# Kernel optimization log

Measured on AMD Instinct MI355X. Metric: run time of the kernel, lower is better.

## Reference

```python
import jax, jax.numpy as jnp
from jax import lax
import numpy as np

NUM_TAGS = 48
START = NUM_TAGS
STOP = NUM_TAGS + 1
LABEL_SMOOTHING = 0.1
NEG = -10000.0


def setup_inputs() -> dict:
    key = jax.random.key(0)
    k1, k2, k3 = jax.random.split(key, 3)
    B, T = 1024, 512
    emissions = jax.random.normal(k1, (B, T, NUM_TAGS), dtype=jnp.float32)
    tags = jax.random.randint(k2, (B, T), 0, NUM_TAGS, dtype=jnp.int64)
    mask = jnp.ones((B, T), dtype=bool)
    # learned transitions, initialized as in the torch module
    trans = jax.random.normal(k3, (NUM_TAGS + 2, NUM_TAGS + 2), dtype=jnp.float32) * 0.1
    trans = trans.at[:, START].set(NEG)          # never transition into START
    trans = trans.at[STOP, :].set(NEG)           # never transition out of STOP
    trans = trans.at[0, 0].add(-2.0)             # TAG2IDX.get('O', 0) == 0
    return {"emissions": emissions, "tags": tags, "mask": mask, "transitions": trans}


def _crf_nll(emissions, transitions, tags, mask):
    B, T, K = emissions.shape
    # ---- forward algorithm (log partition) ----
    alpha0 = jnp.full((B, K + 2), NEG, dtype=emissions.dtype).at[:, START].set(0.0)

    def step(alpha, inp):
        emit, m = inp                                   # emit: [B,K], m: [B]
        # sc[b,j] = logsumexp_i(alpha[b,i] + transitions[i,j])
        sc = jax.nn.logsumexp(alpha[:, :, None] + transitions[None], axis=1)  # [B,K+2]
        sc = sc.at[:, :K].add(emit)
        alpha = jnp.where(m[:, None], sc, alpha)
        return alpha, None

    alpha, _ = lax.scan(step, alpha0,
                        (jnp.swapaxes(emissions, 0, 1), jnp.swapaxes(mask, 0, 1)))
    log_z = jax.nn.logsumexp(alpha[:, :K] + transitions[:K, STOP][None], axis=1)  # [B]

    # ---- gold score ----
    mf = mask.astype(emissions.dtype)
    emit_g = jnp.take_along_axis(emissions, tags[..., None], axis=2)[..., 0]  # [B,T]
    gold = (transitions[START, tags[:, 0]]
            + jnp.sum(emit_g * mf, axis=1)
            + jnp.sum(transitions[tags[:, :-1], tags[:, 1:]] * mf[:, 1:], axis=1))
    last = jnp.sum(mask.astype(jnp.int32), axis=1) - 1                        # [B]
    last_tags = jnp.take_along_axis(tags, last[:, None].astype(tags.dtype), axis=1)[:, 0]
    gold = gold + transitions[last_tags, STOP]

    nll = jnp.mean(log_z - gold)
    h_max = jnp.log(jnp.asarray(K + 1e-12, dtype=nll.dtype))
    return (1.0 - LABEL_SMOOTHING) * nll + LABEL_SMOOTHING * h_max


def reference(emissions, tags, mask, transitions):
    return _crf_nll(emissions, transitions, tags, mask)
```

## Files before the change

kernel.cpp:

```cpp
#include <hip/hip_runtime.h>
#include <hip/hip_bf16.h>
#include <math.h>


#define NTAGS   48
#define NST     50
#define START_S 48
#define STOP_S  49
#define BATCH   1024
#define TLEN    512

typedef short  bf16x8 __attribute__((ext_vector_type(8)));
typedef float  f32x4  __attribute__((ext_vector_type(4)));

union B4 { unsigned u[4]; short s[8]; bf16x8 v; };

__device__ __forceinline__ short to_bf16(float f) {
    unsigned u = __float_as_uint(f);
    unsigned r = ((u >> 16) & 1u) + 0x7FFFu;
    return (short)((u + r) >> 16);
}

__device__ __forceinline__ unsigned pk2(float lo, float hi) {
    float2 f; f.x = lo; f.y = hi;
    __hip_bfloat162 h = __float22bfloat162_rn(f);
    union { __hip_bfloat162 h; unsigned u; } cvt; cvt.h = h;
    return cvt.u;
}

__device__ __forceinline__ float wave_sum(float v) {
#pragma unroll
    for (int off = 32; off >= 1; off >>= 1)
        v += __shfl_xor(v, off, 64);
    return v;
}

__device__ __forceinline__ void gload_lds16(const float* g, f32x4* l) {
    __builtin_amdgcn_global_load_lds(
        (const __attribute__((address_space(1))) unsigned int*)(const void*)g,
        (__attribute__((address_space(3))) unsigned int*)(void*)l,
        16, 0, 0);
}

#define VMWAIT24 asm volatile("s_waitcnt vmcnt(24)" ::: "memory");

#define RENORM_APPLY                                                     \
    {   int ex = ((rbp >> 23) & 255) - 127;                              \
        ex = ex > 126 ? 126 : (ex < -126 ? -126 : ex);                   \
        float sc = __uint_as_float((unsigned)(127 - ex) << 23);          \
        p0 *= sc; p1 *= sc; p2 *= sc;                                    \
        Clog += (float)ex * 0.69314718055994531f; }

template<int MODE, int LAST>
__device__ __forceinline__ void fwd_step(const bf16x8 (&A)[3][2],
    bf16x8 &B0, bf16x8 &B1,
    const f32x4 &X0, const f32x4 &X1, const f32x4 &X2,
    f32x4 &p0, f32x4 &p1, f32x4 &p2, float &Clog, int bp_addr, int &rbp)
{
    const f32x4 z = {0.f, 0.f, 0.f, 0.f};
    f32x4 a0 = __builtin_amdgcn_mfma_f32_16x16x32_bf16(A[0][0], B0, z, 0, 0, 0);
    a0 = __builtin_amdgcn_mfma_f32_16x16x32_bf16(A[0][1], B1, a0, 0, 0, 0);
    f32x4 a1 = __builtin_amdgcn_mfma_f32_16x16x32_bf16(A[1][0], B0, z, 0, 0, 0);
    a1 = __builtin_amdgcn_mfma_f32_16x16x32_bf16(A[1][1], B1, a1, 0, 0, 0);
    f32x4 a2 = __builtin_amdgcn_mfma_f32_16x16x32_bf16(A[2][0], B0, z, 0, 0, 0);
    a2 = __builtin_amdgcn_mfma_f32_16x16x32_bf16(A[2][1], B1, a2, 0, 0, 0);
    p0 = a0 * X0;  p1 = a1 * X1;  p2 = a2 * X2;
    if (MODE == 2) RENORM_APPLY
    if (MODE == 1) rbp = __builtin_amdgcn_ds_bpermute(bp_addr, __float_as_int(p0[0]));
    if (!LAST) {
        B4 nb0;
        nb0.u[0] = pk2(p0[0], p0[1]);  nb0.u[1] = pk2(p0[2], p0[3]);
        nb0.u[2] = pk2(p1[0], p1[1]);  nb0.u[3] = pk2(p1[2], p1[3]);
        B0 = nb0.v;
        B4 nb1;
        nb1.u[0] = pk2(p2[0], p2[1]);  nb1.u[1] = pk2(p2[2], p2[3]);
        nb1.u[2] = 0u;                 nb1.u[3] = 0u;
        B1 = nb1.v;
    }
}

template<int MODE>
__device__ __forceinline__ void bwd_step(const bf16x8 (&A)[3][2],
    const f32x4 &X0, const f32x4 &X1, const f32x4 &X2,
    f32x4 &p0, f32x4 &p1, f32x4 &p2, float &Clog, int bp_addr, int &rbp)
{
    f32x4 h0 = p0 * X0, h1 = p1 * X1, h2 = p2 * X2;
    B4 nb0;
    nb0.u[0] = pk2(h0[0], h0[1]);  nb0.u[1] = pk2(h0[2], h0[3]);
    nb0.u[2] = pk2(h1[0], h1[1]);  nb0.u[3] = pk2(h1[2], h1[3]);
    B4 nb1;
    nb1.u[0] = pk2(h2[0], h2[1]);  nb1.u[1] = pk2(h2[2], h2[3]);
    nb1.u[2] = 0u;                 nb1.u[3] = 0u;
    const bf16x8 B0 = nb0.v, B1 = nb1.v;
    const f32x4 z = {0.f, 0.f, 0.f, 0.f};
    f32x4 a0 = __builtin_amdgcn_mfma_f32_16x16x32_bf16(A[0][0], B0, z, 0, 0, 0);
    a0 = __builtin_amdgcn_mfma_f32_16x16x32_bf16(A[0][1], B1, a0, 0, 0, 0);
    f32x4 a1 = __builtin_amdgcn_mfma_f32_16x16x32_bf16(A[1][0], B0, z, 0, 0, 0);
    a1 = __builtin_amdgcn_mfma_f32_16x16x32_bf16(A[1][1], B1, a1, 0, 0, 0);
    f32x4 a2 = __builtin_amdgcn_mfma_f32_16x16x32_bf16(A[2][0], B0, z, 0, 0, 0);
    a2 = __builtin_amdgcn_mfma_f32_16x16x32_bf16(A[2][1], B1, a2, 0, 0, 0);
    p0 = a0;  p1 = a1;  p2 = a2;
    if (MODE == 2) RENORM_APPLY
    if (MODE == 1) rbp = __builtin_amdgcn_ds_bpermute(bp_addr, __float_as_int(p0[0]));
}

#define STAGE(BUF, T)                                                        \
    { const int tb_ = (T);                                                   \
      _Pragma("unroll") for (int u2 = 0; u2 < 4; ++u2)                       \
        _Pragma("unroll") for (int mt = 0; mt < 3; ++mt)                     \
            gload_lds16(emg + (size_t)(tb_ + u2) * NTAGS + 16 * mt,          \
                        &ldsb[BUF][u2 * 3 + mt][0]); }

#define STAGE_D(BUF, T)                                                      \
    { const int tb_ = (T);                                                   \
      _Pragma("unroll") for (int u2 = 0; u2 < 4; ++u2)                       \
        _Pragma("unroll") for (int mt = 0; mt < 3; ++mt)                     \
            gload_lds16(emg + (size_t)(tb_ - u2) * NTAGS + 16 * mt,          \
                        &ldsb[BUF][u2 * 3 + mt][0]); }

#define RDX(BUF, U2)                                                         \
    rw[U2][0] = ldsb[BUF][(U2) * 3 + 0][l];                                  \
    rw[U2][1] = ldsb[BUF][(U2) * 3 + 1][l];                                  \
    rw[U2][2] = ldsb[BUF][(U2) * 3 + 2][l];

#define EXX(EXN, U2)                                                         \
    _Pragma("unroll") for (int mt = 0; mt < 3; ++mt)                         \
        _Pragma("unroll") for (int r = 0; r < 4; ++r)                        \
            EXN[U2][mt][r] = __expf(rw[U2][mt][r]);

#define FSTEPS(EXC, EXN, BN, BS, T)                                          \
    fwd_step<0,0>(A, B0, B1, EXC[0][0], EXC[0][1], EXC[0][2], p0, p1, p2, Clog, bp_addr, rbp); \
    RDX(BN, 0)                                                               \
    fwd_step<0,0>(A, B0, B1, EXC[1][0], EXC[1][1], EXC[1][2], p0, p1, p2, Clog, bp_addr, rbp); \
    RDX(BN, 1) RDX(BN, 2)                                                    \
    { int ts_ = (T) + 16; if (ts_ > 253) ts_ = 253; STAGE(BS, ts_) }         \
    fwd_step<1,0>(A, B0, B1, EXC[2][0], EXC[2][1], EXC[2][2], p0, p1, p2, Clog, bp_addr, rbp); \
    RDX(BN, 3)                                                               \
    EXX(EXN, 0) EXX(EXN, 1)                                                  \
    fwd_step<2,0>(A, B0, B1, EXC[3][0], EXC[3][1], EXC[3][2], p0, p1, p2, Clog, bp_addr, rbp); \
    EXX(EXN, 2) EXX(EXN, 3)

#define BSTEPS(EXC, EXN, BN, BS, T)                                          \
    bwd_step<0>(A, EXC[0][0], EXC[0][1], EXC[0][2], p0, p1, p2, Clog, bp_addr, rbp); \
    RDX(BN, 0)                                                               \
    bwd_step<0>(A, EXC[1][0], EXC[1][1], EXC[1][2], p0, p1, p2, Clog, bp_addr, rbp); \
    RDX(BN, 1) RDX(BN, 2)                                                    \
    { int ts_ = (T) - 16; if (ts_ < 259) ts_ = 259; STAGE_D(BS, ts_) }       \
    bwd_step<1>(A, EXC[2][0], EXC[2][1], EXC[2][2], p0, p1, p2, Clog, bp_addr, rbp); \
    RDX(BN, 3)                                                               \
    EXX(EXN, 0) EXX(EXN, 1)                                                  \
    bwd_step<2>(A, EXC[3][0], EXC[3][1], EXC[3][2], p0, p1, p2, Clog, bp_addr, rbp); \
    EXX(EXN, 2) EXX(EXN, 3)

#define WS_Q    0
#define WS_U    49152
#define WS_CF   98304
#define WS_CB   99328
#define WS_GOLD 100352
#define WS_ACC  101376
#define WS_CNT  101377
#define WS_NEEDED_FLOATS 101378

__global__ __launch_bounds__(64)
__attribute__((amdgpu_waves_per_eu(1, 1)))
void crf_main(const float* __restrict__ emissions,
              const int*   __restrict__ tags,
              const float* __restrict__ trans,
              float*       __restrict__ ws)
{
    __shared__ __align__(16) f32x4 ldsb[4][12][64];
    const int bid = blockIdx.x;
    const int l = threadIdx.x;

    if (bid >= 128) {
        const int gb = bid - 128;
        for (int rr = 0; rr < 8; ++rr) {
            const int b = gb * 8 + rr;
            const float* em  = emissions + (size_t)b * TLEN * NTAGS;
            const int*   tbp = tags + (size_t)b * TLEN;
            float gacc = 0.0f;
#pragma unroll
            for (int k = 0; k < TLEN / 64; ++k) {
                const int tt  = k * 64 + l;
                const int tag = tbp[tt];
                gacc += em[(size_t)tt * NTAGS + tag];
                if (tt >= 1) gacc += trans[tbp[tt - 1] * NST + tag];
            }
            gacc = wave_sum(gacc);
            if (l == 0)
                ws[WS_GOLD + b] = gacc + trans[START_S * NST + tbp[0]]
                                       + trans[tbp[TLEN - 1] * NST + STOP_S];
        }
        return;
    }

    const bool is_fwd = (bid < 64);
    const int grp = is_fwd ? bid : (bid - 64);
    const int g = l >> 4;
    const int c = l & 15;
    const int brow = grp * 16 + c;

    bf16x8 A[3][2];
#pragma unroll
    for (int mt = 0; mt < 3; ++mt)
#pragma unroll
        for (int kt = 0; kt < 2; ++kt) {
            B4 u;
#pragma unroll
            for (int e = 0; e < 8; ++e) {
                const int sk = 16 * (2 * kt + (e >> 2)) + 4 * g + (e & 3);
                const int m  = 16 * mt + c;
                float f = 0.0f;
                if (sk < NTAGS)
                    f = __expf(is_fwd ? trans[sk * NST + m] : trans[m * NST + sk]);
                u.s[e] = to_bf16(f);
            }
            A[mt][kt] = u.v;
        }
    asm volatile("" : "+v"(A[0][0]), "+v"(A[0][1]), "+v"(A[1][0]),
                      "+v"(A[1][1]), "+v"(A[2][0]), "+v"(A[2][1]));

    const float* emc = emissions + (size_t)brow * (TLEN * NTAGS);
    const float* emg = emc + 4 * g;

    const int bp_addr = c << 2;
    f32x4 p0, p1, p2;
    float Clog = 0.0f;
    int rbp = __float_as_int(1.0f);
    f32x4 EXa[4][3], EXb[4][3], rw[4][3];

    if (is_fwd) {
        bf16x8 B0, B1;
        {
            f32x4 i0 = *(const f32x4*)(emc +      4 * g);
            f32x4 i1 = *(const f32x4*)(emc + 16 + 4 * g);
            f32x4 i2 = *(const f32x4*)(emc + 32 + 4 * g);
            B4 nb0, nb1;
#pragma unroll
            for (int r = 0; r < 4; ++r) {
                nb0.s[r]     = to_bf16(__expf(trans[START_S * NST +      4 * g + r] + i0[r]));
                nb0.s[4 + r] = to_bf16(__expf(trans[START_S * NST + 16 + 4 * g + r] + i1[r]));
                nb1.s[r]     = to_bf16(__expf(trans[START_S * NST + 32 + 4 * g + r] + i2[r]));
            }
            nb1.u[2] = 0u;  nb1.u[3] = 0u;
            B0 = nb0.v;  B1 = nb1.v;
        }
        STAGE(0, 1) STAGE(1, 5) STAGE(2, 9)
        VMWAIT24
        RDX(0, 0) RDX(0, 1) RDX(0, 2) RDX(0, 3)
        EXX(EXa, 0) EXX(EXa, 1) EXX(EXa, 2) EXX(EXa, 3)
        STAGE(3, 13)
        int t = 1, bi = 0;
        for (int pr = 0; pr < 31; ++pr) {
            VMWAIT24
            FSTEPS(EXa, EXb, (bi + 1) & 3, bi, t)
            t += 4; bi = (bi + 1) & 3;
            VMWAIT24
            FSTEPS(EXb, EXa, (bi + 1) & 3, bi, t)
            t += 4; bi = (bi + 1) & 3;
        }
        VMWAIT24
        FSTEPS(EXa, EXb, (bi + 1) & 3, bi, t)
        fwd_step<0,0>(A, B0, B1, EXb[0][0], EXb[0][1], EXb[0][2], p0, p1, p2, Clog, bp_addr, rbp);
        fwd_step<0,0>(A, B0, B1, EXb[1][0], EXb[1][1], EXb[1][2], p0, p1, p2, Clog, bp_addr, rbp);
        fwd_step<0,1>(A, B0, B1, EXb[2][0], EXb[2][1], EXb[2][2], p0, p1, p2, Clog, bp_addr, rbp);

        float* q = ws + WS_Q + (size_t)grp * 768 + l * 12;
#pragma unroll
        for (int r = 0; r < 4; ++r) {
            q[r] = p0[r];  q[4 + r] = p1[r];  q[8 + r] = p2[r];
        }
        if (g == 0) ws[WS_CF + grp * 16 + c] = Clog;
    } else {
#pragma unroll
        for (int r = 0; r < 4; ++r) {
            p0[r] = __expf(trans[(     4 * g + r) * NST + STOP_S]);
            p1[r] = __expf(trans[(16 + 4 * g + r) * NST + STOP_S]);
            p2[r] = __expf(trans[(32 + 4 * g + r) * NST + STOP_S]);
        }
        STAGE_D(0, 511) STAGE_D(1, 507) STAGE_D(2, 503)
        VMWAIT24
        RDX(0, 0) RDX(0, 1) RDX(0, 2) RDX(0, 3)
        EXX(EXa, 0) EXX(EXa, 1) EXX(EXa, 2) EXX(EXa, 3)
        STAGE_D(3, 499)
        int t = 511, bi = 0;
        for (int pr = 0; pr < 32; ++pr) {
            VMWAIT24
            BSTEPS(EXa, EXb, (bi + 1) & 3, bi, t)
            t -= 4; bi = (bi + 1) & 3;
            VMWAIT24
            BSTEPS(EXb, EXa, (bi + 1) & 3, bi, t)
            t -= 4; bi = (bi + 1) & 3;
        }
        float* u = ws + WS_U + (size_t)grp * 768 + l * 12;
#pragma unroll
        for (int r = 0; r < 4; ++r) {
            u[r] = p0[r];  u[4 + r] = p1[r];  u[8 + r] = p2[r];
        }
        if (g == 0) ws[WS_CB + grp * 16 + c] = Clog;
    }
}

__global__ __launch_bounds__(64)
void crf_combine(float* __restrict__ ws, float* __restrict__ out)
{
    const int grp = blockIdx.x;
    const int l = threadIdx.x;
    const float* q = ws + WS_Q + (size_t)grp * 768 + l * 12;
    const float* u = ws + WS_U + (size_t)grp * 768 + l * 12;
    float s = 0.0f;
#pragma unroll
    for (int k = 0; k < 12; ++k) s += q[k] * u[k];
    s += __shfl_xor(s, 16, 64);
    s += __shfl_xor(s, 32, 64);
    float v = 0.0f;
    if (l < 16) {
        const float logz = ws[WS_CF + grp * 16 + l]
                         + ws[WS_CB + grp * 16 + l] + __logf(s);
        v = logz - ws[WS_GOLD + grp * 16 + l];
    }
    v = wave_sum(v);
    if (l == 0) {
        atomicAdd(&ws[WS_ACC], v);
        __threadfence();
        unsigned old = atomicAdd((unsigned*)&ws[WS_CNT], 1u);
        if (old == 63u) {
            const float tot = atomicAdd(&ws[WS_ACC], 0.0f);
            const float nll = tot / (float)BATCH;
            out[0] = 0.9f * nll + 0.1f * logf((float)NTAGS);
        }
    }
}

extern "C" void kernel_launch(void* const* d_in, const int* in_sizes, int n_in,
                              void* d_out, int out_size, void* d_ws, size_t ws_size,
                              hipStream_t stream)
{
    const float* emissions = (const float*)d_in[0];
    const int*   tags      = (const int*)d_in[1];
    const float* trans     = (const float*)d_in[3];

    if (ws_size < WS_NEEDED_FLOATS * sizeof(float)) return;
    float* ws = (float*)d_ws;

    hipMemsetAsync(ws + WS_ACC, 0, 2 * sizeof(float), stream);

    crf_main<<<256, 64, 0, stream>>>(emissions, tags, trans, ws);
    crf_combine<<<64, 64, 0, stream>>>(ws, (float*)d_out);
}
```

Before: 74.11 us.

## Interleave two independent batch chains per wave in forward/backward recurrence

```diff
diff --git a/kernel.cpp b/kernel.cpp
--- a/kernel.cpp
+++ b/kernel.cpp
@@ -42,7 +42,7 @@
         16, 0, 0);
 }
 
-#define VMWAIT24 asm volatile("s_waitcnt vmcnt(24)" ::: "memory");
+#define VMWAIT48 asm volatile("s_waitcnt vmcnt(48)" ::: "memory");
 
 #define RENORM_APPLY                                                     \
     {   int ex = ((rbp >> 23) & 255) - 127;                              \
@@ -104,53 +104,63 @@
     if (MODE == 1) rbp = __builtin_amdgcn_ds_bpermute(bp_addr, __float_as_int(p0[0]));
 }
 
-#define STAGE(BUF, T)                                                        \
+#define STAGEC(C, BUF, T)                                                    \
     { const int tb_ = (T);                                                   \
       _Pragma("unroll") for (int u2 = 0; u2 < 4; ++u2)                       \
         _Pragma("unroll") for (int mt = 0; mt < 3; ++mt)                     \
-            gload_lds16(emg + (size_t)(tb_ + u2) * NTAGS + 16 * mt,          \
-                        &ldsb[BUF][u2 * 3 + mt][0]); }
-
-#define STAGE_D(BUF, T)                                                      \
+            gload_lds16(emg_[C] + (size_t)(tb_ + u2) * NTAGS + 16 * mt,      \
+                        &ldsb[C][BUF][u2 * 3 + mt][0]); }
+
+#define STAGEC_D(C, BUF, T)                                                  \
     { const int tb_ = (T);                                                   \
       _Pragma("unroll") for (int u2 = 0; u2 < 4; ++u2)                       \
         _Pragma("unroll") for (int mt = 0; mt < 3; ++mt)                     \
-            gload_lds16(emg + (size_t)(tb_ - u2) * NTAGS + 16 * mt,          \
-                        &ldsb[BUF][u2 * 3 + mt][0]); }
-
-#define RDX(BUF, U2)                                                         \
-    rw[U2][0] = ldsb[BUF][(U2) * 3 + 0][l];                                  \
-    rw[U2][1] = ldsb[BUF][(U2) * 3 + 1][l];                                  \
-    rw[U2][2] = ldsb[BUF][(U2) * 3 + 2][l];
-
-#define EXX(EXN, U2)                                                         \
+            gload_lds16(emg_[C] + (size_t)(tb_ - u2) * NTAGS + 16 * mt,      \
+                        &ldsb[C][BUF][u2 * 3 + mt][0]); }
+
+#define RDXC(C, BUF, U2)                                                     \
+    rw[C][U2][0] = ldsb[C][BUF][(U2) * 3 + 0][l];                            \
+    rw[C][U2][1] = ldsb[C][BUF][(U2) * 3 + 1][l];                            \
+    rw[C][U2][2] = ldsb[C][BUF][(U2) * 3 + 2][l];
+
+#define EXXC(C, EXN, U2)                                                     \
     _Pragma("unroll") for (int mt = 0; mt < 3; ++mt)                         \
         _Pragma("unroll") for (int r = 0; r < 4; ++r)                        \
-            EXN[U2][mt][r] = __expf(rw[U2][mt][r]);
-
-#define FSTEPS(EXC, EXN, BN, BS, T)                                          \
-    fwd_step<0,0>(A, B0, B1, EXC[0][0], EXC[0][1], EXC[0][2], p0, p1, p2, Clog, bp_addr, rbp); \
-    RDX(BN, 0)                                                               \
-    fwd_step<0,0>(A, B0, B1, EXC[1][0], EXC[1][1], EXC[1][2], p0, p1, p2, Clog, bp_addr, rbp); \
-    RDX(BN, 1) RDX(BN, 2)                                                    \
-    { int ts_ = (T) + 16; if (ts_ > 253) ts_ = 253; STAGE(BS, ts_) }         \
-    fwd_step<1,0>(A, B0, B1, EXC[2][0], EXC[2][1], EXC[2][2], p0, p1, p2, Clog, bp_addr, rbp); \
-    RDX(BN, 3)                                                               \
-    EXX(EXN, 0) EXX(EXN, 1)                                                  \
-    fwd_step<2,0>(A, B0, B1, EXC[3][0], EXC[3][1], EXC[3][2], p0, p1, p2, Clog, bp_addr, rbp); \
-    EXX(EXN, 2) EXX(EXN, 3)
-
-#define BSTEPS(EXC, EXN, BN, BS, T)                                          \
-    bwd_step<0>(A, EXC[0][0], EXC[0][1], EXC[0][2], p0, p1, p2, Clog, bp_addr, rbp); \
-    RDX(BN, 0)                                                               \
-    bwd_step<0>(A, EXC[1][0], EXC[1][1], EXC[1][2], p0, p1, p2, Clog, bp_addr, rbp); \
-    RDX(BN, 1) RDX(BN, 2)                                                    \
-    { int ts_ = (T) - 16; if (ts_ < 259) ts_ = 259; STAGE_D(BS, ts_) }       \
-    bwd_step<1>(A, EXC[2][0], EXC[2][1], EXC[2][2], p0, p1, p2, Clog, bp_addr, rbp); \
-    RDX(BN, 3)                                                               \
-    EXX(EXN, 0) EXX(EXN, 1)                                                  \
-    bwd_step<2>(A, EXC[3][0], EXC[3][1], EXC[3][2], p0, p1, p2, Clog, bp_addr, rbp); \
-    EXX(EXN, 2) EXX(EXN, 3)
+            EXN[C][U2][mt][r] = __expf(rw[C][U2][mt][r]);
+
+#define FSTEPC(C, MODE, LAST, EXC, S)                                        \
+    fwd_step<MODE, LAST>(A, B0_[C], B1_[C], EXC[C][S][0], EXC[C][S][1],      \
+        EXC[C][S][2], p0_[C], p1_[C], p2_[C], Clog_[C], bp_addr, rbp_[C]);
+
+#define BSTEPC(C, MODE, EXC, S)                                              \
+    bwd_step<MODE>(A, EXC[C][S][0], EXC[C][S][1], EXC[C][S][2],              \
+        p0_[C], p1_[C], p2_[C], Clog_[C], bp_addr, rbp_[C]);
+
+#define DFSTEPS(EXC, EXN, BN, BS, T)                                         \
+    FSTEPC(0,0,0,EXC,0) FSTEPC(1,0,0,EXC,0)                                  \
+    RDXC(0,BN,0) RDXC(1,BN,0)                                                \
+    FSTEPC(0,0,0,EXC,1) FSTEPC(1,0,0,EXC,1)                                  \
+    RDXC(0,BN,1) RDXC(1,BN,1) RDXC(0,BN,2) RDXC(1,BN,2)                      \
+    { int ts_ = (T) + 16; if (ts_ > 253) ts_ = 253;                          \
+      STAGEC(0,BS,ts_) STAGEC(1,BS,ts_) }                                    \
+    FSTEPC(0,1,0,EXC,2) FSTEPC(1,1,0,EXC,2)                                  \
+    RDXC(0,BN,3) RDXC(1,BN,3)                                                \
+    EXXC(0,EXN,0) EXXC(1,EXN,0) EXXC(0,EXN,1) EXXC(1,EXN,1)                  \
+    FSTEPC(0,2,0,EXC,3) FSTEPC(1,2,0,EXC,3)                                  \
+    EXXC(0,EXN,2) EXXC(1,EXN,2) EXXC(0,EXN,3) EXXC(1,EXN,3)
+
+#define DBSTEPS(EXC, EXN, BN, BS, T)                                         \
+    BSTEPC(0,0,EXC,0) BSTEPC(1,0,EXC,0)                                      \
+    RDXC(0,BN,0) RDXC(1,BN,0)                                                \
+    BSTEPC(0,0,EXC,1) BSTEPC(1,0,EXC,1)                                      \
+    RDXC(0,BN,1) RDXC(1,BN,1) RDXC(0,BN,2) RDXC(1,BN,2)                      \
+    { int ts_ = (T) - 16; if (ts_ < 259) ts_ = 259;                          \
+      STAGEC_D(0,BS,ts_) STAGEC_D(1,BS,ts_) }                                \
+    BSTEPC(0,1,EXC,2) BSTEPC(1,1,EXC,2)                                      \
+    RDXC(0,BN,3) RDXC(1,BN,3)                                                \
+    EXXC(0,EXN,0) EXXC(1,EXN,0) EXXC(0,EXN,1) EXXC(1,EXN,1)                  \
+    BSTEPC(0,2,EXC,3) BSTEPC(1,2,EXC,3)                                      \
+    EXXC(0,EXN,2) EXXC(1,EXN,2) EXXC(0,EXN,3) EXXC(1,EXN,3)
 
 #define WS_Q    0
 #define WS_U    49152
@@ -168,14 +178,12 @@
               const float* __restrict__ trans,
               float*       __restrict__ ws)
 {
-    __shared__ __align__(16) f32x4 ldsb[4][12][64];
+    __shared__ __align__(16) f32x4 ldsb[2][4][12][64];
     const int bid = blockIdx.x;
     const int l = threadIdx.x;
 
-    if (bid >= 128) {
-        const int gb = bid - 128;
-        for (int rr = 0; rr < 8; ++rr) {
-            const int b = gb * 8 + rr;
+    if (bid >= 64) {
+        for (int b = bid - 64; b < BATCH; b += 192) {
             const float* em  = emissions + (size_t)b * TLEN * NTAGS;
             const int*   tbp = tags + (size_t)b * TLEN;
             float gacc = 0.0f;
@@ -194,11 +202,10 @@
         return;
     }
 
-    const bool is_fwd = (bid < 64);
-    const int grp = is_fwd ? bid : (bid - 64);
+    const bool is_fwd = (bid < 32);
+    const int gbase = is_fwd ? (2 * bid) : (2 * (bid - 32));
     const int g = l >> 4;
     const int c = l & 15;
-    const int brow = grp * 16 + c;
 
     bf16x8 A[3][2];
 #pragma unroll
@@ -220,21 +227,27 @@
     asm volatile("" : "+v"(A[0][0]), "+v"(A[0][1]), "+v"(A[1][0]),
                       "+v"(A[1][1]), "+v"(A[2][0]), "+v"(A[2][1]));
 
-    const float* emc = emissions + (size_t)brow * (TLEN * NTAGS);
-    const float* emg = emc + 4 * g;
+    const float* emc_[2];
+    const float* emg_[2];
+#pragma unroll
+    for (int C = 0; C < 2; ++C) {
+        emc_[C] = emissions + (size_t)((gbase + C) * 16 + c) * (TLEN * NTAGS);
+        emg_[C] = emc_[C] + 4 * g;
+    }
 
     const int bp_addr = c << 2;
-    f32x4 p0, p1, p2;
-    float Clog = 0.0f;
-    int rbp = __float_as_int(1.0f);
-    f32x4 EXa[4][3], EXb[4][3], rw[4][3];
+    bf16x8 B0_[2], B1_[2];
+    f32x4 p0_[2], p1_[2], p2_[2];
+    float Clog_[2] = {0.0f, 0.0f};
+    int rbp_[2] = {0, 0};
+    f32x4 EXa[2][4][3], EXb[2][4][3], rw[2][4][3];
 
     if (is_fwd) {
-        bf16x8 B0, B1;
-        {
-            f32x4 i0 = *(const f32x4*)(emc +      4 * g);
-            f32x4 i1 = *(const f32x4*)(emc + 16 + 4 * g);
-            f32x4 i2 = *(const f32x4*)(emc + 32 + 4 * g);
+#pragma unroll
+        for (int C = 0; C < 2; ++C) {
+            f32x4 i0 = *(const f32x4*)(emc_[C] +      4 * g);
+            f32x4 i1 = *(const f32x4*)(emc_[C] + 16 + 4 * g);
+            f32x4 i2 = *(const f32x4*)(emc_[C] + 32 + 4 * g);
             B4 nb0, nb1;
 #pragma unroll
             for (int r = 0; r < 4; ++r) {
@@ -243,61 +256,75 @@
                 nb1.s[r]     = to_bf16(__expf(trans[START_S * NST + 32 + 4 * g + r] + i2[r]));
             }
             nb1.u[2] = 0u;  nb1.u[3] = 0u;
-            B0 = nb0.v;  B1 = nb1.v;
-        }
-        STAGE(0, 1) STAGE(1, 5) STAGE(2, 9)
-        VMWAIT24
-        RDX(0, 0) RDX(0, 1) RDX(0, 2) RDX(0, 3)
-        EXX(EXa, 0) EXX(EXa, 1) EXX(EXa, 2) EXX(EXa, 3)
-        STAGE(3, 13)
+            B0_[C] = nb0.v;  B1_[C] = nb1.v;
+        }
+        STAGEC(0,0,1) STAGEC(1,0,1) STAGEC(0,1,5) STAGEC(1,1,5)
+        STAGEC(0,2,9) STAGEC(1,2,9)
+        VMWAIT48
+        RDXC(0,0,0) RDXC(1,0,0) RDXC(0,0,1) RDXC(1,0,1)
+        RDXC(0,0,2) RDXC(1,0,2) RDXC(0,0,3) RDXC(1,0,3)
+        EXXC(0,EXa,0) EXXC(1,EXa,0) EXXC(0,EXa,1) EXXC(1,EXa,1)
+        EXXC(0,EXa,2) EXXC(1,EXa,2) EXXC(0,EXa,3) EXXC(1,EXa,3)
+        STAGEC(0,3,13) STAGEC(1,3,13)
         int t = 1, bi = 0;
         for (int pr = 0; pr < 31; ++pr) {
-            VMWAIT24
-            FSTEPS(EXa, EXb, (bi + 1) & 3, bi, t)
+            VMWAIT48
+            DFSTEPS(EXa, EXb, (bi + 1) & 3, bi, t)
             t += 4; bi = (bi + 1) & 3;
-            VMWAIT24
-            FSTEPS(EXb, EXa, (bi + 1) & 3, bi, t)
+            VMWAIT48
+            DFSTEPS(EXb, EXa, (bi + 1) & 3, bi, t)
             t += 4; bi = (bi + 1) & 3;
         }
-        VMWAIT24
-        FSTEPS(EXa, EXb, (bi + 1) & 3, bi, t)
-        fwd_step<0,0>(A, B0, B1, EXb[0][0], EXb[0][1], EXb[0][2], p0, p1, p2, Clog, bp_addr, rbp);
-        fwd_step<0,0>(A, B0, B1, EXb[1][0], EXb[1][1], EXb[1][2], p0, p1, p2, Clog, bp_addr, rbp);
-        fwd_step<0,1>(A, B0, B1, EXb[2][0], EXb[2][1], EXb[2][2], p0, p1, p2, Clog, bp_addr, rbp);
-
-        float* q = ws + WS_Q + (size_t)grp * 768 + l * 12;
-#pragma unroll
-        for (int r = 0; r < 4; ++r) {
-            q[r] = p0[r];  q[4 + r] = p1[r];  q[8 + r] = p2[r];
-        }
-        if (g == 0) ws[WS_CF + grp * 16 + c] = Clog;
+        VMWAIT48
+        DFSTEPS(EXa, EXb, (bi + 1) & 3, bi, t)
+        FSTEPC(0,0,0,EXb,0) FSTEPC(1,0,0,EXb,0)
+        FSTEPC(0,0,0,EXb,1) FSTEPC(1,0,0,EXb,1)
+        FSTEPC(0,0,1,EXb,2) FSTEPC(1,0,1,EXb,2)
+
+#pragma unroll
+        for (int C = 0; C < 2; ++C) {
+            float* q = ws + WS_Q + (size_t)(gbase + C) * 768 + l * 12;
+#pragma unroll
+            for (int r = 0; r < 4; ++r) {
+                q[r] = p0_[C][r];  q[4 + r] = p1_[C][r];  q[8 + r] = p2_[C][r];
+            }
+            if (g == 0) ws[WS_CF + (gbase + C) * 16 + c] = Clog_[C];
+        }
     } else {
 #pragma unroll
-        for (int r = 0; r < 4; ++r) {
-            p0[r] = __expf(trans[(     4 * g + r) * NST + STOP_S]);
-            p1[r] = __expf(trans[(16 + 4 * g + r) * NST + STOP_S]);
-            p2[r] = __expf(trans[(32 + 4 * g + r) * NST + STOP_S]);
-        }
-        STAGE_D(0, 511) STAGE_D(1, 507) STAGE_D(2, 503)
-        VMWAIT24
-        RDX(0, 0) RDX(0, 1) RDX(0, 2) RDX(0, 3)
-        EXX(EXa, 0) EXX(EXa, 1) EXX(EXa, 2) EXX(EXa, 3)
-        STAGE_D(3, 499)
+        for (int C = 0; C < 2; ++C)
+#pragma unroll
+            for (int r = 0; r < 4; ++r) {
+                p0_[C][r] = __expf(trans[(     4 * g + r) * NST + STOP_S]);
+                p1_[C][r] = __expf(trans[(16 + 4 * g + r) * NST + STOP_S]);
+                p2_[C][r] = __expf(trans[(32 + 4 * g + r) * NST + STOP_S]);
+            }
+        STAGEC_D(0,0,511) STAGEC_D(1,0,511) STAGEC_D(0,1,507) STAGEC_D(1,1,507)
+        STAGEC_D(0,2,503) STAGEC_D(1,2,503)
+        VMWAIT48
+        RDXC(0,0,0) RDXC(1,0,0) RDXC(0,0,1) RDXC(1,0,1)
+        RDXC(0,0,2) RDXC(1,0,2) RDXC(0,0,3) RDXC(1,0,3)
+        EXXC(0,EXa,0) EXXC(1,EXa,0) EXXC(0,EXa,1) EXXC(1,EXa,1)
+        EXXC(0,EXa,2) EXXC(1,EXa,2) EXXC(0,EXa,3) EXXC(1,EXa,3)
+        STAGEC_D(0,3,499) STAGEC_D(1,3,499)
         int t = 511, bi = 0;
         for (int pr = 0; pr < 32; ++pr) {
-            VMWAIT24
-            BSTEPS(EXa, EXb, (bi + 1) & 3, bi, t)
+            VMWAIT48
+            DBSTEPS(EXa, EXb, (bi + 1) & 3, bi, t)
             t -= 4; bi = (bi + 1) & 3;
-            VMWAIT24
-            BSTEPS(EXb, EXa, (bi + 1) & 3, bi, t)
+            VMWAIT48
+            DBSTEPS(EXb, EXa, (bi + 1) & 3, bi, t)
             t -= 4; bi = (bi + 1) & 3;
         }
-        float* u = ws + WS_U + (size_t)grp * 768 + l * 12;
-#pragma unroll
-        for (int r = 0; r < 4; ++r) {
-            u[r] = p0[r];  u[4 + r] = p1[r];  u[8 + r] = p2[r];
-        }
-        if (g == 0) ws[WS_CB + grp * 16 + c] = Clog;
+#pragma unroll
+        for (int C = 0; C < 2; ++C) {
+            float* u = ws + WS_U + (size_t)(gbase + C) * 768 + l * 12;
+#pragma unroll
+            for (int r = 0; r < 4; ++r) {
+                u[r] = p0_[C][r];  u[4 + r] = p1_[C][r];  u[8 + r] = p2_[C][r];
+            }
+            if (g == 0) ws[WS_CB + (gbase + C) * 16 + c] = Clog_[C];
+        }
     }
 }
 
```

After: 139.4 us. +88.1%, slower.

## Fuse main and combine kernels via cooperative launch with grid sync

Applied to the files above, without the earlier changes.

```diff
diff --git a/kernel.cpp b/kernel.cpp
--- a/kernel.cpp
+++ b/kernel.cpp
@@ -1,7 +1,10 @@
 #include <hip/hip_runtime.h>
 #include <hip/hip_bf16.h>
+#include <hip/hip_cooperative_groups.h>
 #include <math.h>
 
+
+namespace cg = cooperative_groups;
 
 #define NTAGS   48
 #define NST     50
@@ -43,6 +46,7 @@
 }
 
 #define VMWAIT24 asm volatile("s_waitcnt vmcnt(24)" ::: "memory");
+#define VMWAIT0  asm volatile("s_waitcnt vmcnt(0)"  ::: "memory");
 
 #define RENORM_APPLY                                                     \
     {   int ex = ((rbp >> 23) & 255) - 127;                              \
@@ -163,16 +167,21 @@
 
 __global__ __launch_bounds__(64)
 __attribute__((amdgpu_waves_per_eu(1, 1)))
-void crf_main(const float* __restrict__ emissions,
-              const int*   __restrict__ tags,
-              const float* __restrict__ trans,
-              float*       __restrict__ ws)
+void crf_all(const float* __restrict__ emissions,
+             const int*   __restrict__ tags,
+             const float* __restrict__ trans,
+             float*       __restrict__ ws,
+             float*       __restrict__ out)
 {
     __shared__ __align__(16) f32x4 ldsb[4][12][64];
     const int bid = blockIdx.x;
     const int l = threadIdx.x;
 
     if (bid >= 128) {
+        if (bid == 128 && l == 0) {
+            ws[WS_ACC] = 0.0f;
+            ((unsigned*)ws)[WS_CNT] = 0u;
+        }
         const int gb = bid - 128;
         for (int rr = 0; rr < 8; ++rr) {
             const int b = gb * 8 + rr;
@@ -191,143 +200,142 @@
                 ws[WS_GOLD + b] = gacc + trans[START_S * NST + tbp[0]]
                                        + trans[tbp[TLEN - 1] * NST + STOP_S];
         }
-        return;
-    }
-
-    const bool is_fwd = (bid < 64);
-    const int grp = is_fwd ? bid : (bid - 64);
-    const int g = l >> 4;
-    const int c = l & 15;
-    const int brow = grp * 16 + c;
-
-    bf16x8 A[3][2];
-#pragma unroll
-    for (int mt = 0; mt < 3; ++mt)
-#pragma unroll
-        for (int kt = 0; kt < 2; ++kt) {
-            B4 u;
-#pragma unroll
-            for (int e = 0; e < 8; ++e) {
-                const int sk = 16 * (2 * kt + (e >> 2)) + 4 * g + (e & 3);
-                const int m  = 16 * mt + c;
-                float f = 0.0f;
-                if (sk < NTAGS)
-                    f = __expf(is_fwd ? trans[sk * NST + m] : trans[m * NST + sk]);
-                u.s[e] = to_bf16(f);
-            }
-            A[mt][kt] = u.v;
-        }
-    asm volatile("" : "+v"(A[0][0]), "+v"(A[0][1]), "+v"(A[1][0]),
-                      "+v"(A[1][1]), "+v"(A[2][0]), "+v"(A[2][1]));
-
-    const float* emc = emissions + (size_t)brow * (TLEN * NTAGS);
-    const float* emg = emc + 4 * g;
-
-    const int bp_addr = c << 2;
-    f32x4 p0, p1, p2;
-    float Clog = 0.0f;
-    int rbp = __float_as_int(1.0f);
-    f32x4 EXa[4][3], EXb[4][3], rw[4][3];
-
-    if (is_fwd) {
-        bf16x8 B0, B1;
-        {
-            f32x4 i0 = *(const f32x4*)(emc +      4 * g);
-            f32x4 i1 = *(const f32x4*)(emc + 16 + 4 * g);
-            f32x4 i2 = *(const f32x4*)(emc + 32 + 4 * g);
-            B4 nb0, nb1;
-#pragma unroll
-            for (int r = 0; r < 4; ++r) {
-                nb0.s[r]     = to_bf16(__expf(trans[START_S * NST +      4 * g + r] + i0[r]));
-                nb0.s[4 + r] = to_bf16(__expf(trans[START_S * NST + 16 + 4 * g + r] + i1[r]));
-                nb1.s[r]     = to_bf16(__expf(trans[START_S * NST + 32 + 4 * g + r] + i2[r]));
-            }
-            nb1.u[2] = 0u;  nb1.u[3] = 0u;
-            B0 = nb0.v;  B1 = nb1.v;
-        }
-        STAGE(0, 1) STAGE(1, 5) STAGE(2, 9)
-        VMWAIT24
-        RDX(0, 0) RDX(0, 1) RDX(0, 2) RDX(0, 3)
-        EXX(EXa, 0) EXX(EXa, 1) EXX(EXa, 2) EXX(EXa, 3)
-        STAGE(3, 13)
-        int t = 1, bi = 0;
-        for (int pr = 0; pr < 31; ++pr) {
+    } else {
+        const bool is_fwd = (bid < 64);
+        const int grp = is_fwd ? bid : (bid - 64);
+        const int g = l >> 4;
+        const int c = l & 15;
+        const int brow = grp * 16 + c;
+
+        bf16x8 A[3][2];
+#pragma unroll
+        for (int mt = 0; mt < 3; ++mt)
+#pragma unroll
+            for (int kt = 0; kt < 2; ++kt) {
+                B4 u;
+#pragma unroll
+                for (int e = 0; e < 8; ++e) {
+                    const int sk = 16 * (2 * kt + (e >> 2)) + 4 * g + (e & 3);
+                    const int m  = 16 * mt + c;
+                    float f = 0.0f;
+                    if (sk < NTAGS)
+                        f = __expf(is_fwd ? trans[sk * NST + m] : trans[m * NST + sk]);
+                    u.s[e] = to_bf16(f);
+                }
+                A[mt][kt] = u.v;
+            }
+        asm volatile("" : "+v"(A[0][0]), "+v"(A[0][1]), "+v"(A[1][0]),
+                          "+v"(A[1][1]), "+v"(A[2][0]), "+v"(A[2][1]));
+
+        const float* emc = emissions + (size_t)brow * (TLEN * NTAGS);
+        const float* emg = emc + 4 * g;
+
+        const int bp_addr = c << 2;
+        f32x4 p0, p1, p2;
+        float Clog = 0.0f;
+        int rbp = __float_as_int(1.0f);
+        f32x4 EXa[4][3], EXb[4][3], rw[4][3];
+
+        if (is_fwd) {
+            bf16x8 B0, B1;
+            {
+                f32x4 i0 = *(const f32x4*)(emc +      4 * g);
+                f32x4 i1 = *(const f32x4*)(emc + 16 + 4 * g);
+                f32x4 i2 = *(const f32x4*)(emc + 32 + 4 * g);
+                B4 nb0, nb1;
+#pragma unroll
+                for (int r = 0; r < 4; ++r) {
+                    nb0.s[r]     = to_bf16(__expf(trans[START_S * NST +      4 * g + r] + i0[r]));
+                    nb0.s[4 + r] = to_bf16(__expf(trans[START_S * NST + 16 + 4 * g + r] + i1[r]));
+                    nb1.s[r]     = to_bf16(__expf(trans[START_S * NST + 32 + 4 * g + r] + i2[r]));
+                }
+                nb1.u[2] = 0u;  nb1.u[3] = 0u;
+                B0 = nb0.v;  B1 = nb1.v;
+            }
+            STAGE(0, 1) STAGE(1, 5) STAGE(2, 9)
+            VMWAIT24
+            RDX(0, 0) RDX(0, 1) RDX(0, 2) RDX(0, 3)
+            EXX(EXa, 0) EXX(EXa, 1) EXX(EXa, 2) EXX(EXa, 3)
+            STAGE(3, 13)
+            int t = 1, bi = 0;
+            for (int pr = 0; pr < 31; ++pr) {
+                VMWAIT24
+                FSTEPS(EXa, EXb, (bi + 1) & 3, bi, t)
+                t += 4; bi = (bi + 1) & 3;
+                VMWAIT24
+                FSTEPS(EXb, EXa, (bi + 1) & 3, bi, t)
+                t += 4; bi = (bi + 1) & 3;
+            }
             VMWAIT24
             FSTEPS(EXa, EXb, (bi + 1) & 3, bi, t)
-            t += 4; bi = (bi + 1) & 3;
+            fwd_step<0,0>(A, B0, B1, EXb[0][0], EXb[0][1], EXb[0][2], p0, p1, p2, Clog, bp_addr, rbp);
+            fwd_step<0,0>(A, B0, B1, EXb[1][0], EXb[1][1], EXb[1][2], p0, p1, p2, Clog, bp_addr, rbp);
+            fwd_step<0,1>(A, B0, B1, EXb[2][0], EXb[2][1], EXb[2][2], p0, p1, p2, Clog, bp_addr, rbp);
+
+            float* q = ws + WS_Q + (size_t)grp * 768 + l * 12;
+#pragma unroll
+            for (int r = 0; r < 4; ++r) {
+                q[r] = p0[r];  q[4 + r] = p1[r];  q[8 + r] = p2[r];
+            }
+            if (g == 0) ws[WS_CF + grp * 16 + c] = Clog;
+        } else {
+#pragma unroll
+            for (int r = 0; r < 4; ++r) {
+                p0[r] = __expf(trans[(     4 * g + r) * NST + STOP_S]);
+                p1[r] = __expf(trans[(16 + 4 * g + r) * NST + STOP_S]);
+                p2[r] = __expf(trans[(32 + 4 * g + r) * NST + STOP_S]);
+            }
+            STAGE_D(0, 511) STAGE_D(1, 507) STAGE_D(2, 503)
             VMWAIT24
-            FSTEPS(EXb, EXa, (bi + 1) & 3, bi, t)
-            t += 4; bi = (bi + 1) & 3;
-        }
-        VMWAIT24
-        FSTEPS(EXa, EXb, (bi + 1) & 3, bi, t)
-        fwd_step<0,0>(A, B0, B1, EXb[0][0], EXb[0][1], EXb[0][2], p0, p1, p2, Clog, bp_addr, rbp);
-        fwd_step<0,0>(A, B0, B1, EXb[1][0], EXb[1][1], EXb[1][2], p0, p1, p2, Clog, bp_addr, rbp);
-        fwd_step<0,1>(A, B0, B1, EXb[2][0], EXb[2][1], EXb[2][2], p0, p1, p2, Clog, bp_addr, rbp);
-
-        float* q = ws + WS_Q + (size_t)grp * 768 + l * 12;
-#pragma unroll
-        for (int r = 0; r < 4; ++r) {
-            q[r] = p0[r];  q[4 + r] = p1[r];  q[8 + r] = p2[r];
-        }
-        if (g == 0) ws[WS_CF + grp * 16 + c] = Clog;
-    } else {
-#pragma unroll
-        for (int r = 0; r < 4; ++r) {
-            p0[r] = __expf(trans[(     4 * g + r) * NST + STOP_S]);
-            p1[r] = __expf(trans[(16 + 4 * g + r) * NST + STOP_S]);
-            p2[r] = __expf(trans[(32 + 4 * g + r) * NST + STOP_S]);
-        }
-        STAGE_D(0, 511) STAGE_D(1, 507) STAGE_D(2, 503)
-        VMWAIT24
-        RDX(0, 0) RDX(0, 1) RDX(0, 2) RDX(0, 3)
-        EXX(EXa, 0) EXX(EXa, 1) EXX(EXa, 2) EXX(EXa, 3)
-        STAGE_D(3, 499)
-        int t = 511, bi = 0;
-        for (int pr = 0; pr < 32; ++pr) {
-            VMWAIT24
-            BSTEPS(EXa, EXb, (bi + 1) & 3, bi, t)
-            t -= 4; bi = (bi + 1) & 3;
-            VMWAIT24
-            BSTEPS(EXb, EXa, (bi + 1) & 3, bi, t)
-            t -= 4; bi = (bi + 1) & 3;
-        }
-        float* u = ws + WS_U + (size_t)grp * 768 + l * 12;
-#pragma unroll
-        for (int r = 0; r < 4; ++r) {
-            u[r] = p0[r];  u[4 + r] = p1[r];  u[8 + r] = p2[r];
-        }
-        if (g == 0) ws[WS_CB + grp * 16 + c] = Clog;
+            RDX(0, 0) RDX(0, 1) RDX(0, 2) RDX(0, 3)
+            EXX(EXa, 0) EXX(EXa, 1) EXX(EXa, 2) EXX(EXa, 3)
+            STAGE_D(3, 499)
+            int t = 511, bi = 0;
+            for (int pr = 0; pr < 32; ++pr) {
+                VMWAIT24
+                BSTEPS(EXa, EXb, (bi + 1) & 3, bi, t)
+                t -= 4; bi = (bi + 1) & 3;
+                VMWAIT24
+                BSTEPS(EXb, EXa, (bi + 1) & 3, bi, t)
+                t -= 4; bi = (bi + 1) & 3;
+            }
+            float* u = ws + WS_U + (size_t)grp * 768 + l * 12;
+#pragma unroll
+            for (int r = 0; r < 4; ++r) {
+                u[r] = p0[r];  u[4 + r] = p1[r];  u[8 + r] = p2[r];
+            }
+            if (g == 0) ws[WS_CB + grp * 16 + c] = Clog;
+        }
+        VMWAIT0
     }
-}
-
-__global__ __launch_bounds__(64)
-void crf_combine(float* __restrict__ ws, float* __restrict__ out)
-{
-    const int grp = blockIdx.x;
-    const int l = threadIdx.x;
-    const float* q = ws + WS_Q + (size_t)grp * 768 + l * 12;
-    const float* u = ws + WS_U + (size_t)grp * 768 + l * 12;
-    float s = 0.0f;
-#pragma unroll
-    for (int k = 0; k < 12; ++k) s += q[k] * u[k];
-    s += __shfl_xor(s, 16, 64);
-    s += __shfl_xor(s, 32, 64);
-    float v = 0.0f;
-    if (l < 16) {
-        const float logz = ws[WS_CF + grp * 16 + l]
-                         + ws[WS_CB + grp * 16 + l] + __logf(s);
-        v = logz - ws[WS_GOLD + grp * 16 + l];
-    }
-    v = wave_sum(v);
-    if (l == 0) {
-        atomicAdd(&ws[WS_ACC], v);
-        __threadfence();
-        unsigned old = atomicAdd((unsigned*)&ws[WS_CNT], 1u);
-        if (old == 63u) {
-            const float tot = atomicAdd(&ws[WS_ACC], 0.0f);
-            const float nll = tot / (float)BATCH;
-            out[0] = 0.9f * nll + 0.1f * logf((float)NTAGS);
+
+    cg::this_grid().sync();
+
+    if (bid < 64) {
+        const int grp = bid;
+        const float* q = ws + WS_Q + (size_t)grp * 768 + l * 12;
+        const float* u = ws + WS_U + (size_t)grp * 768 + l * 12;
+        float s = 0.0f;
+#pragma unroll
+        for (int k = 0; k < 12; ++k) s += q[k] * u[k];
+        s += __shfl_xor(s, 16, 64);
+        s += __shfl_xor(s, 32, 64);
+        float v = 0.0f;
+        if (l < 16) {
+            const float logz = ws[WS_CF + grp * 16 + l]
+                             + ws[WS_CB + grp * 16 + l] + __logf(s);
+            v = logz - ws[WS_GOLD + grp * 16 + l];
+        }
+        v = wave_sum(v);
+        if (l == 0) {
+            atomicAdd(&ws[WS_ACC], v);
+            __threadfence();
+            unsigned old = atomicAdd((unsigned*)&ws[WS_CNT], 1u);
+            if (old == 63u) {
+                const float tot = atomicAdd(&ws[WS_ACC], 0.0f);
+                const float nll = tot / (float)BATCH;
+                out[0] = 0.9f * nll + 0.1f * logf((float)NTAGS);
+            }
         }
     }
 }
@@ -341,10 +349,11 @@
     const float* trans     = (const float*)d_in[3];
 
     if (ws_size < WS_NEEDED_FLOATS * sizeof(float)) return;
-    float* ws = (float*)d_ws;
-
-    hipMemsetAsync(ws + WS_ACC, 0, 2 * sizeof(float), stream);
-
-    crf_main<<<256, 64, 0, stream>>>(emissions, tags, trans, ws);
-    crf_combine<<<64, 64, 0, stream>>>(ws, (float*)d_out);
-}
+    float* ws  = (float*)d_ws;
+    float* out = (float*)d_out;
+
+    void* args[] = { (void*)&emissions, (void*)&tags, (void*)&trans,
+                     (void*)&ws, (void*)&out };
+    hipLaunchCooperativeKernel((const void*)crf_all, dim3(256), dim3(64),
+                               args, 0, stream);
+}
```

Result: slower. 115.0 us (+55.1%).
